# Kernel tuning notes

Measured on AMD Instinct MI355X. Metric: run time of the kernel, lower is better.

Reference implementation:

```python
import jax, jax.numpy as jnp
import numpy as np

IN, H, NCLS = 1280, 128, 263


def _lstm_scan(x_tbd, Wih, Whh, bih, bhh):
    # x_tbd: [T, B, IN]; PyTorch gate order: i, f, g, o. Wih: [4H, IN], Whh: [4H, H]
    B = x_tbd.shape[1]
    b = bih + bhh
    # precompute input projections once: [T, B, 4H]
    xp = jnp.einsum('tbd,gd->tbg', x_tbd, Wih) + b

    def step(carry, xg):
        h, c = carry
        gates = xg + h @ Whh.T
        i, f, g, o = jnp.split(gates, 4, axis=-1)
        i = jax.nn.sigmoid(i)
        f = jax.nn.sigmoid(f)
        g = jnp.tanh(g)
        o = jax.nn.sigmoid(o)
        c = f * c + i * g
        h = o * jnp.tanh(c)
        return (h, c), h

    h0 = jnp.zeros((B, H), x_tbd.dtype)
    c0 = jnp.zeros((B, H), x_tbd.dtype)
    _, hs = jax.lax.scan(step, (h0, c0), xp)
    return hs  # [T, B, H]


def setup_inputs() -> dict:
    key = jax.random.key(0)
    ks = jax.random.split(key, 11)
    s_ih = 1.0 / np.sqrt(H)
    u = lambda k, shape: jax.random.uniform(k, shape, jnp.float32, -s_ih, s_ih)
    return {
        'x': jax.random.normal(ks[0], (64, 512, IN), jnp.float32),
        'Wih_f': u(ks[1], (4 * H, IN)),
        'Whh_f': u(ks[2], (4 * H, H)),
        'bih_f': u(ks[3], (4 * H,)),
        'bhh_f': u(ks[4], (4 * H,)),
        'Wih_b': u(ks[5], (4 * H, IN)),
        'Whh_b': u(ks[6], (4 * H, H)),
        'bih_b': u(ks[7], (4 * H,)),
        'bhh_b': u(ks[8], (4 * H,)),
        'W1': u(ks[9], (NCLS, 2 * H)),
        'b1': u(ks[10], (NCLS,)),
    }


def reference(x, Wih_f, Whh_f, bih_f, bhh_f, Wih_b, Whh_b, bih_b, bhh_b, W1, b1):
    x_tbd = jnp.swapaxes(x, 0, 1)  # [T, B, IN]
    h_f = _lstm_scan(x_tbd, Wih_f, Whh_f, bih_f, bhh_f)           # [T, B, H]
    h_b = _lstm_scan(x_tbd[::-1], Wih_b, Whh_b, bih_b, bhh_b)[::-1]
    h = jnp.concatenate([h_f, h_b], axis=-1)  # [T, B, 2H]
    pooled = jnp.max(h, axis=0)               # temporal max-pool -> [B, 2H]
    # dropout treated as identity (deterministic eval-mode baseline)
    return pooled @ W1.T + b1                  # [B, 263]
```

## Files before the change

kernel.cpp:

```cpp
#include <hip/hip_runtime.h>
#include <hip/hip_bf16.h>

typedef short short8v __attribute__((ext_vector_type(8)));
typedef short short4v __attribute__((ext_vector_type(4)));
typedef float f32x4v __attribute__((ext_vector_type(4)));

#define T_LEN 512
#define BATCH 64
#define INDIM 1280
#define HDIM 128
#define G4 512
#define NCOLS 1024
#define NCLS 263

typedef __attribute__((address_space(1))) const void gvoid_t;
typedef __attribute__((address_space(3))) void lvoid_t;
#define GLOAD_LDS16(g, l) __builtin_amdgcn_global_load_lds((gvoid_t*)(g), (lvoid_t*)(l), 16, 0, 0)

static __device__ __forceinline__ short f2bf(float f) {
    union { float f; unsigned u; } v; v.f = f;
    unsigned r = v.u + 0x7FFF + ((v.u >> 16) & 1);
    return (short)(r >> 16);
}

__global__ void convert_x_kernel(const float4* __restrict__ x, short4v* __restrict__ out, int n4) {
    int i = blockIdx.x * blockDim.x + threadIdx.x;
    int stride = gridDim.x * blockDim.x;
    for (; i < n4; i += stride) {
        float4 v = x[i];
        short4v o;
        o[0] = f2bf(v.x); o[1] = f2bf(v.y); o[2] = f2bf(v.z); o[3] = f2bf(v.w);
        out[i] = o;
    }
}

__global__ void convert_w_kernel(const float* __restrict__ Wf, const float* __restrict__ Wb,
                                 const float* __restrict__ bihf, const float* __restrict__ bhhf,
                                 const float* __restrict__ bihb, const float* __restrict__ bhhb,
                                 short* __restrict__ wout, float* __restrict__ biasc) {
    int i = blockIdx.x * blockDim.x + threadIdx.x;
    int stride = gridDim.x * blockDim.x;
    const int n4 = (G4 * INDIM) / 4;
    for (int k = i; k < 2 * n4; k += stride) {
        const float4* src = (k < n4) ? (const float4*)Wf : (const float4*)Wb;
        float4 v = src[(k < n4) ? k : (k - n4)];
        short4v o;
        o[0] = f2bf(v.x); o[1] = f2bf(v.y); o[2] = f2bf(v.z); o[3] = f2bf(v.w);
        ((short4v*)wout)[k] = o;
    }
    if (i < NCOLS)
        biasc[i] = (i < G4) ? (bihf[i] + bhhf[i]) : (bihb[i - G4] + bhhb[i - G4]);
}

#define BM 128
#define BN 128
#define BK 32

__global__ __launch_bounds__(256) void gemm_xp_kernel(const short* __restrict__ A,
                                                      const short* __restrict__ Bw,
                                                      const float* __restrict__ bias,
                                                      float* __restrict__ C) {
    __shared__ __align__(16) short As[BM * BK];
    __shared__ __align__(16) short Bs[BN * BK];
    const int tid = threadIdx.x;
    const int w = tid >> 6;
    const int l = tid & 63;
    const int bm = blockIdx.x * BM;
    const int bn = blockIdx.y * BN;
    const int wm = (w >> 1) * 64;
    const int wn = (w & 1) * 64;
    const int lr = l & 15;
    const int lk = (l >> 4) * 8;

    f32x4v acc[4][4];
#pragma unroll
    for (int m = 0; m < 4; m++)
#pragma unroll
        for (int n = 0; n < 4; n++) acc[m][n] = (f32x4v)0.0f;

    const int srow = tid >> 2;
    const int scol = (tid & 3) * 8;

#pragma unroll
    for (int i = 0; i < 2; i++) {
        GLOAD_LDS16(A + (long)(bm + i * 64 + srow) * INDIM + scol, &As[(i * 64 + (w << 4)) * BK]);
        GLOAD_LDS16(Bw + (long)(bn + i * 64 + srow) * INDIM + scol, &Bs[(i * 64 + (w << 4)) * BK]);
    }

    for (int k0 = 0; k0 < INDIM; k0 += BK) {
        __syncthreads();
        short8v af[4], bf[4];
#pragma unroll
        for (int m = 0; m < 4; m++) af[m] = *(const short8v*)&As[(wm + m * 16 + lr) * BK + lk];
#pragma unroll
        for (int n = 0; n < 4; n++) bf[n] = *(const short8v*)&Bs[(wn + n * 16 + lr) * BK + lk];
        __syncthreads();
        if (k0 + BK < INDIM) {
            const int k1 = k0 + BK;
#pragma unroll
            for (int i = 0; i < 2; i++) {
                GLOAD_LDS16(A + (long)(bm + i * 64 + srow) * INDIM + k1 + scol, &As[(i * 64 + (w << 4)) * BK]);
                GLOAD_LDS16(Bw + (long)(bn + i * 64 + srow) * INDIM + k1 + scol, &Bs[(i * 64 + (w << 4)) * BK]);
            }
        }
#pragma unroll
        for (int m = 0; m < 4; m++)
#pragma unroll
            for (int n = 0; n < 4; n++)
                acc[m][n] = __builtin_amdgcn_mfma_f32_16x16x32_bf16(af[m], bf[n], acc[m][n], 0, 0, 0);
    }

#pragma unroll
    for (int m = 0; m < 4; m++) {
        const int row = bm + wm + m * 16 + (l >> 4) * 4;
#pragma unroll
        for (int n = 0; n < 4; n++) {
            const int col = bn + wn + n * 16 + lr;
            const float bv = bias[col];
#pragma unroll
            for (int r = 0; r < 4; r++)
                C[(long)(row + r) * NCOLS + col] = acc[m][n][r] + bv;
        }
    }
}

__global__ __launch_bounds__(256, 1) void lstm_rec_kernel(const float* __restrict__ xp,
                                                          const float* __restrict__ Whh_f,
                                                          const float* __restrict__ Whh_b,
                                                          float* __restrict__ pooled) {
    __shared__ __align__(16) short hbf[2][3][136];
    __shared__ __align__(16) float glds[4][2][136];

    const int bid = blockIdx.x;
    const int d = bid & 1;
    const int b0 = (bid >> 1) * 2;
    const int tid = threadIdx.x;
    const int w = tid >> 6;
    const int l = tid & 63;
    const int lr = l & 15;
    const int lg = l >> 4;
    const int lk = lg * 8;
    const int hrow = lr < 2 ? lr : 2;

    const float* __restrict__ Whh = d ? Whh_b : Whh_f;

    short8v afragW[8][4];
#pragma unroll
    for (int nt = 0; nt < 8; nt++) {
        const int gc = w * 128 + nt * 16 + lr;
#pragma unroll
        for (int kk = 0; kk < 4; kk++) {
            const float* src = Whh + gc * HDIM + kk * 32 + lk;
            short8v f;
#pragma unroll
            for (int j = 0; j < 8; j++) f[j] = f2bf(src[j]);
            afragW[nt][kk] = f;
        }
    }

    for (int i = tid; i < 2 * 3 * 136; i += 256) ((short*)hbf)[i] = 0;

    const int eb = tid >> 7;
    const int ec = tid & 127;
    const float* xbase = xp + (long)(b0 + eb) * T_LEN * NCOLS + d * G4 + ec;

    float c = 0.0f;
    float hmax = -1e30f;

#define LOADXV(tq, dst) { \
    int tt_ = d ? (T_LEN - 1 - (tq)) : (tq); \
    tt_ = tt_ < 0 ? 0 : (tt_ > T_LEN - 1 ? T_LEN - 1 : tt_); \
    const float* p_ = xbase + (long)tt_ * NCOLS; \
    _Pragma("unroll") for (int nt_ = 0; nt_ < 4; nt_++) \
        dst[nt_] = p_[nt_ * 128]; \
}

    float xvA[4], xvB[4];
    LOADXV(0, xvA);
    LOADXV(1, xvB);

    __syncthreads();

#define L2E 1.44269504088896f

#define STEP(t, pb, xv) { \
    short8v hfrag[4]; \
    _Pragma("unroll") for (int kk = 0; kk < 4; kk++) \
        hfrag[kk] = *(const short8v*)&hbf[pb][hrow][kk * 32 + lk]; \
    _Pragma("unroll") for (int nt = 0; nt < 8; nt++) { \
        f32x4v a = (f32x4v)0.0f; \
        _Pragma("unroll") for (int kk = 0; kk < 4; kk++) \
            a = __builtin_amdgcn_mfma_f32_16x16x32_bf16(afragW[nt][kk], hfrag[kk], a, 0, 0, 0); \
        if (lr < 2) *(f32x4v*)&glds[w][lr][nt * 16 + lg * 4] = a; \
    } \
    asm volatile("s_waitcnt lgkmcnt(0)\n\ts_barrier" ::: "memory"); \
    { \
        float gi = glds[0][eb][ec] + xv[0]; \
        float gf = glds[1][eb][ec] + xv[1]; \
        float gg = glds[2][eb][ec] + xv[2]; \
        float go = glds[3][eb][ec] + xv[3]; \
        float ea = __builtin_amdgcn_exp2f(-gi * L2E); \
        float eb_ = __builtin_amdgcn_exp2f(-gf * L2E); \
        float pa = 1.0f + ea, pbv = 1.0f + eb_; \
        float inv1 = __builtin_amdgcn_rcpf(pa * pbv); \
        float si = pbv * inv1; \
        float sf = pa * inv1; \
        float eg = __builtin_amdgcn_exp2f(gg * (2.0f * L2E)); \
        float eo = __builtin_amdgcn_exp2f(-go * L2E); \
        float pg = 1.0f + eg, po = 1.0f + eo; \
        float inv2 = __builtin_amdgcn_rcpf(pg * po); \
        float tg = 1.0f - 2.0f * po * inv2; \
        float so = pg * inv2; \
        c = sf * c + si * tg; \
        float ecx = __builtin_amdgcn_exp2f(c * (2.0f * L2E)); \
        float tc = 1.0f - 2.0f * __builtin_amdgcn_rcpf(1.0f + ecx); \
        float h = so * tc; \
        hmax = fmaxf(hmax, h); \
        hbf[(pb) ^ 1][eb][ec] = f2bf(h); \
    } \
    LOADXV((t) + 2, xv); \
    asm volatile("s_waitcnt lgkmcnt(0)\n\ts_barrier" ::: "memory"); \
}

    for (int t = 0; t < T_LEN; t += 2) {
        STEP(t, 0, xvA);
        STEP(t + 1, 1, xvB);
    }

    pooled[(b0 + eb) * 256 + d * 128 + ec] = hmax;
#undef STEP
#undef LOADXV
}

__global__ void logits_kernel(const float* __restrict__ pooled, const float* __restrict__ W1,
                              const float* __restrict__ b1, float* __restrict__ out) {
    __shared__ float p[256];
    const int b = blockIdx.x;
    const int n = threadIdx.x;
    if (n < 256) p[n] = pooled[b * 256 + n];
    __syncthreads();
    if (n < NCLS) {
        float s = b1[n];
        const float* wr = W1 + n * 256;
#pragma unroll 8
        for (int k = 0; k < 256; k++) s += p[k] * wr[k];
        out[b * NCLS + n] = s;
    }
}

extern "C" void kernel_launch(void* const* d_in, const int* in_sizes, int n_in,
                              void* d_out, int out_size, void* d_ws, size_t ws_size,
                              hipStream_t stream) {
    (void)in_sizes; (void)n_in; (void)out_size; (void)ws_size;
    const float* x     = (const float*)d_in[0];
    const float* Wih_f = (const float*)d_in[1];
    const float* Whh_f = (const float*)d_in[2];
    const float* bih_f = (const float*)d_in[3];
    const float* bhh_f = (const float*)d_in[4];
    const float* Wih_b = (const float*)d_in[5];
    const float* Whh_b = (const float*)d_in[6];
    const float* bih_b = (const float*)d_in[7];
    const float* bhh_b = (const float*)d_in[8];
    const float* W1    = (const float*)d_in[9];
    const float* b1    = (const float*)d_in[10];
    float* out = (float*)d_out;

    char* ws = (char*)d_ws;
    short* x_bf   = (short*)ws;
    short* w_bf   = (short*)(ws + 83886080);
    float* biasc  = (float*)(ws + 86507520);
    float* xp     = (float*)(ws + 86511616);
    float* pooled = (float*)(ws + 220729344);

    convert_x_kernel<<<2048, 256, 0, stream>>>((const float4*)x, (short4v*)x_bf, (T_LEN * BATCH * INDIM) / 4);
    convert_w_kernel<<<512, 256, 0, stream>>>(Wih_f, Wih_b, bih_f, bhh_f, bih_b, bhh_b, w_bf, biasc);
    dim3 g(BATCH * T_LEN / BM, NCOLS / BN);
    gemm_xp_kernel<<<g, 256, 0, stream>>>(x_bf, w_bf, biasc, xp);
    lstm_rec_kernel<<<64, 256, 0, stream>>>(xp, Whh_f, Whh_b, pooled);
    logits_kernel<<<64, 320, 0, stream>>>(pooled, W1, b1, out);
}
```

Measured before the change: 504.6 us.

## Remap recurrent gate columns per wave to drop mid-step block barrier

Reassigns the Whh gate columns so that each wave computes all four gates (i,f,g,o) for its own 32 hidden units. The elementwise cell update can then read gate values written by the same wave, and the block-wide barrier between the MFMA phase and the activation phase is removed. The MFMA loop is also reordered to interleave eight independent accumulators across k, which hides MFMA dependency latency. The risk is correctness: intra-wave LDS write-then-read now depends on implicit wave ordering and lgkmcnt waits with no explicit fence.

```diff
diff --git a/kernel.cpp b/kernel.cpp
--- a/kernel.cpp
+++ b/kernel.cpp
@@ -129,7 +129,7 @@
                                                           const float* __restrict__ Whh_b,
                                                           float* __restrict__ pooled) {
     __shared__ __align__(16) short hbf[2][3][136];
-    __shared__ __align__(16) float glds[4][2][136];
+    __shared__ __align__(16) float gw[4][4][2][32];
 
     const int bid = blockIdx.x;
     const int d = bid & 1;
@@ -147,7 +147,7 @@
     short8v afragW[8][4];
 #pragma unroll
     for (int nt = 0; nt < 8; nt++) {
-        const int gc = w * 128 + nt * 16 + lr;
+        const int gc = (nt & 3) * 128 + w * 32 + (nt >> 2) * 16 + lr;
 #pragma unroll
         for (int kk = 0; kk < 4; kk++) {
             const float* src = Whh + gc * HDIM + kk * 32 + lk;
@@ -160,12 +160,14 @@
 
     for (int i = tid; i < 2 * 3 * 136; i += 256) ((short*)hbf)[i] = 0;
 
-    const int eb = tid >> 7;
-    const int ec = tid & 127;
+    const int eb = l >> 5;
+    const int ecl = l & 31;
+    const int ec = w * 32 + ecl;
     const float* xbase = xp + (long)(b0 + eb) * T_LEN * NCOLS + d * G4 + ec;
 
     float c = 0.0f;
     float hmax = -1e30f;
+    const f32x4v z4 = (f32x4v)0.0f;
 
 #define LOADXV(tq, dst) { \
     int tt_ = d ? (T_LEN - 1 - (tq)) : (tq); \
@@ -187,18 +189,21 @@
     short8v hfrag[4]; \
     _Pragma("unroll") for (int kk = 0; kk < 4; kk++) \
         hfrag[kk] = *(const short8v*)&hbf[pb][hrow][kk * 32 + lk]; \
-    _Pragma("unroll") for (int nt = 0; nt < 8; nt++) { \
-        f32x4v a = (f32x4v)0.0f; \
-        _Pragma("unroll") for (int kk = 0; kk < 4; kk++) \
-            a = __builtin_amdgcn_mfma_f32_16x16x32_bf16(afragW[nt][kk], hfrag[kk], a, 0, 0, 0); \
-        if (lr < 2) *(f32x4v*)&glds[w][lr][nt * 16 + lg * 4] = a; \
+    f32x4v acc[8]; \
+    _Pragma("unroll") for (int nt = 0; nt < 8; nt++) \
+        acc[nt] = __builtin_amdgcn_mfma_f32_16x16x32_bf16(afragW[nt][0], hfrag[0], z4, 0, 0, 0); \
+    _Pragma("unroll") for (int kk = 1; kk < 4; kk++) \
+        _Pragma("unroll") for (int nt = 0; nt < 8; nt++) \
+            acc[nt] = __builtin_amdgcn_mfma_f32_16x16x32_bf16(afragW[nt][kk], hfrag[kk], acc[nt], 0, 0, 0); \
+    if (lr < 2) { \
+        _Pragma("unroll") for (int nt = 0; nt < 8; nt++) \
+            *(f32x4v*)&gw[w][nt & 3][lr][(nt >> 2) * 16 + lg * 4] = acc[nt]; \
     } \
-    asm volatile("s_waitcnt lgkmcnt(0)\n\ts_barrier" ::: "memory"); \
     { \
-        float gi = glds[0][eb][ec] + xv[0]; \
-        float gf = glds[1][eb][ec] + xv[1]; \
-        float gg = glds[2][eb][ec] + xv[2]; \
-        float go = glds[3][eb][ec] + xv[3]; \
+        float gi = gw[w][0][eb][ecl] + xv[0]; \
+        float gf = gw[w][1][eb][ecl] + xv[1]; \
+        float gg = gw[w][2][eb][ecl] + xv[2]; \
+        float go = gw[w][3][eb][ecl] + xv[3]; \
         float ea = __builtin_amdgcn_exp2f(-gi * L2E); \
         float eb_ = __builtin_amdgcn_exp2f(-gf * L2E); \
         float pa = 1.0f + ea, pbv = 1.0f + eb_; \
```

Result: no change. 513.1 us (+1.7%).

## Fuse input-projection GEMM with LSTM recurrence using per-tile readiness flags

Applied to the files above, without the earlier changes.

Merges the xp GEMM and the recurrent LSTM kernel into one launch. The first 64 blocks run the recurrence, and the remaining blocks compute GEMM tiles in a time-ordered schedule. Each GEMM block publishes a release-atomic flag when its tile is done. Recurrence blocks poll these flags every 64 steps for the upcoming time window, so the serial recurrence can start before the whole GEMM finishes. The risks are spin-wait overhead, and deadlock or stalls if the recurrence blocks occupy CUs while GEMM tiles are not scheduled. It also adds a memset launch for the flags.

```diff
diff --git a/kernel.cpp b/kernel.cpp
--- a/kernel.cpp
+++ b/kernel.cpp
@@ -56,80 +56,94 @@
 #define BN 128
 #define BK 32
 
-__global__ __launch_bounds__(256) void gemm_xp_kernel(const short* __restrict__ A,
-                                                      const short* __restrict__ Bw,
-                                                      const float* __restrict__ bias,
-                                                      float* __restrict__ C) {
-    __shared__ __align__(16) short As[BM * BK];
-    __shared__ __align__(16) short Bs[BN * BK];
-    const int tid = threadIdx.x;
-    const int w = tid >> 6;
-    const int l = tid & 63;
-    const int bm = blockIdx.x * BM;
-    const int bn = blockIdx.y * BN;
-    const int wm = (w >> 1) * 64;
-    const int wn = (w & 1) * 64;
-    const int lr = l & 15;
-    const int lk = (l >> 4) * 8;
-
-    f32x4v acc[4][4];
-#pragma unroll
-    for (int m = 0; m < 4; m++)
-#pragma unroll
-        for (int n = 0; n < 4; n++) acc[m][n] = (f32x4v)0.0f;
-
-    const int srow = tid >> 2;
-    const int scol = (tid & 3) * 8;
-
-#pragma unroll
-    for (int i = 0; i < 2; i++) {
-        GLOAD_LDS16(A + (long)(bm + i * 64 + srow) * INDIM + scol, &As[(i * 64 + (w << 4)) * BK]);
-        GLOAD_LDS16(Bw + (long)(bn + i * 64 + srow) * INDIM + scol, &Bs[(i * 64 + (w << 4)) * BK]);
-    }
-
-    for (int k0 = 0; k0 < INDIM; k0 += BK) {
-        __syncthreads();
-        short8v af[4], bf[4];
-#pragma unroll
-        for (int m = 0; m < 4; m++) af[m] = *(const short8v*)&As[(wm + m * 16 + lr) * BK + lk];
-#pragma unroll
-        for (int n = 0; n < 4; n++) bf[n] = *(const short8v*)&Bs[(wn + n * 16 + lr) * BK + lk];
-        __syncthreads();
-        if (k0 + BK < INDIM) {
-            const int k1 = k0 + BK;
-#pragma unroll
-            for (int i = 0; i < 2; i++) {
-                GLOAD_LDS16(A + (long)(bm + i * 64 + srow) * INDIM + k1 + scol, &As[(i * 64 + (w << 4)) * BK]);
-                GLOAD_LDS16(Bw + (long)(bn + i * 64 + srow) * INDIM + k1 + scol, &Bs[(i * 64 + (w << 4)) * BK]);
+__global__ __launch_bounds__(256, 1) void fused_gemm_rec_kernel(
+    const short* __restrict__ A, const short* __restrict__ Bw,
+    const float* __restrict__ biasv, float* __restrict__ xp,
+    const float* __restrict__ Whh_f, const float* __restrict__ Whh_b,
+    float* __restrict__ pooled, int* __restrict__ flags) {
+    __shared__ __align__(16) char smem[16384];
+
+    if (blockIdx.x >= 64) {
+        short* As = (short*)smem;
+        short* Bs = (short*)(smem + 8192);
+        const int gid = blockIdx.x - 64;
+        const int chunk = gid >> 8;
+        const int within = gid & 255;
+        const int half = chunk & 1;
+        const int qi = half ? (3 - (chunk >> 1)) : (chunk >> 1);
+        const int gx = (within >> 2) * 4 + qi;
+        const int gy = half * 4 + (within & 3);
+        const int bm = gx * BM;
+        const int bn = gy * BN;
+
+        const int tid = threadIdx.x;
+        const int w = tid >> 6;
+        const int l = tid & 63;
+        const int wm = (w >> 1) * 64;
+        const int wn = (w & 1) * 64;
+        const int lr = l & 15;
+        const int lk = (l >> 4) * 8;
+
+        f32x4v acc[4][4];
+#pragma unroll
+        for (int m = 0; m < 4; m++)
+#pragma unroll
+            for (int n = 0; n < 4; n++) acc[m][n] = (f32x4v)0.0f;
+
+        const int srow = tid >> 2;
+        const int scol = (tid & 3) * 8;
+
+#pragma unroll
+        for (int i = 0; i < 2; i++) {
+            GLOAD_LDS16(A + (long)(bm + i * 64 + srow) * INDIM + scol, &As[(i * 64 + (w << 4)) * BK]);
+            GLOAD_LDS16(Bw + (long)(bn + i * 64 + srow) * INDIM + scol, &Bs[(i * 64 + (w << 4)) * BK]);
+        }
+
+        for (int k0 = 0; k0 < INDIM; k0 += BK) {
+            __syncthreads();
+            short8v af[4], bf[4];
+#pragma unroll
+            for (int m = 0; m < 4; m++) af[m] = *(const short8v*)&As[(wm + m * 16 + lr) * BK + lk];
+#pragma unroll
+            for (int n = 0; n < 4; n++) bf[n] = *(const short8v*)&Bs[(wn + n * 16 + lr) * BK + lk];
+            __syncthreads();
+            if (k0 + BK < INDIM) {
+                const int k1 = k0 + BK;
+#pragma unroll
+                for (int i = 0; i < 2; i++) {
+                    GLOAD_LDS16(A + (long)(bm + i * 64 + srow) * INDIM + k1 + scol, &As[(i * 64 + (w << 4)) * BK]);
+                    GLOAD_LDS16(Bw + (long)(bn + i * 64 + srow) * INDIM + k1 + scol, &Bs[(i * 64 + (w << 4)) * BK]);
+                }
+            }
+#pragma unroll
+            for (int m = 0; m < 4; m++)
+#pragma unroll
+                for (int n = 0; n < 4; n++)
+                    acc[m][n] = __builtin_amdgcn_mfma_f32_16x16x32_bf16(af[m], bf[n], acc[m][n], 0, 0, 0);
+        }
+
+#pragma unroll
+        for (int m = 0; m < 4; m++) {
+            const int row = bm + wm + m * 16 + (l >> 4) * 4;
+#pragma unroll
+            for (int n = 0; n < 4; n++) {
+                const int col = bn + wn + n * 16 + lr;
+                const float bv = biasv[col];
+#pragma unroll
+                for (int r = 0; r < 4; r++)
+                    xp[(long)(row + r) * NCOLS + col] = acc[m][n][r] + bv;
             }
         }
-#pragma unroll
-        for (int m = 0; m < 4; m++)
-#pragma unroll
-            for (int n = 0; n < 4; n++)
-                acc[m][n] = __builtin_amdgcn_mfma_f32_16x16x32_bf16(af[m], bf[n], acc[m][n], 0, 0, 0);
-    }
-
-#pragma unroll
-    for (int m = 0; m < 4; m++) {
-        const int row = bm + wm + m * 16 + (l >> 4) * 4;
-#pragma unroll
-        for (int n = 0; n < 4; n++) {
-            const int col = bn + wn + n * 16 + lr;
-            const float bv = bias[col];
-#pragma unroll
-            for (int r = 0; r < 4; r++)
-                C[(long)(row + r) * NCOLS + col] = acc[m][n][r] + bv;
-        }
-    }
-}
-
-__global__ __launch_bounds__(256, 1) void lstm_rec_kernel(const float* __restrict__ xp,
-                                                          const float* __restrict__ Whh_f,
-                                                          const float* __restrict__ Whh_b,
-                                                          float* __restrict__ pooled) {
-    __shared__ __align__(16) short hbf[2][3][136];
-    __shared__ __align__(16) float glds[4][2][136];
+
+        __threadfence();
+        __syncthreads();
+        if (threadIdx.x == 0)
+            __hip_atomic_fetch_add(&flags[gx * 2 + half], 1, __ATOMIC_RELEASE, __HIP_MEMORY_SCOPE_AGENT);
+        return;
+    }
+
+    short (*hbf)[3][136] = (short (*)[3][136])smem;
+    float (*glds)[2][136] = (float (*)[2][136])(smem + 1632);
 
     const int bid = blockIdx.x;
     const int d = bid & 1;
@@ -158,7 +172,7 @@
         }
     }
 
-    for (int i = tid; i < 2 * 3 * 136; i += 256) ((short*)hbf)[i] = 0;
+    for (int i = tid; i < 2 * 3 * 136; i += 256) ((short*)smem)[i] = 0;
 
     const int eb = tid >> 7;
     const int ec = tid & 127;
@@ -166,6 +180,20 @@
 
     float c = 0.0f;
     float hmax = -1e30f;
+
+#define POLL_WINDOW(t) { \
+    int lo_ = d ? (T_LEN - 1 - (t) - 65) : (t); \
+    int hi_ = d ? (T_LEN - 1 - (t)) : ((t) + 65); \
+    lo_ = lo_ < 0 ? 0 : lo_; hi_ = hi_ > T_LEN - 1 ? T_LEN - 1 : hi_; \
+    const int qa_ = lo_ >> 7, qb_ = hi_ >> 7; \
+    for (int q_ = qa_; q_ <= qb_; ++q_) { \
+        const int f0_ = ((b0) * 4 + q_) * 2 + d; \
+        const int f1_ = ((b0 + 1) * 4 + q_) * 2 + d; \
+        while (__hip_atomic_load(&flags[f0_], __ATOMIC_ACQUIRE, __HIP_MEMORY_SCOPE_AGENT) < 4 || \
+               __hip_atomic_load(&flags[f1_], __ATOMIC_ACQUIRE, __HIP_MEMORY_SCOPE_AGENT) < 4) \
+            __builtin_amdgcn_s_sleep(8); \
+    } \
+}
 
 #define LOADXV(tq, dst) { \
     int tt_ = d ? (T_LEN - 1 - (tq)) : (tq); \
@@ -174,6 +202,8 @@
     _Pragma("unroll") for (int nt_ = 0; nt_ < 4; nt_++) \
         dst[nt_] = p_[nt_ * 128]; \
 }
+
+    POLL_WINDOW(0);
 
     float xvA[4], xvB[4];
     LOADXV(0, xvA);
@@ -223,6 +253,7 @@
 }
 
     for (int t = 0; t < T_LEN; t += 2) {
+        if (t && ((t & 63) == 0)) POLL_WINDOW(t);
         STEP(t, 0, xvA);
         STEP(t + 1, 1, xvB);
     }
@@ -230,6 +261,7 @@
     pooled[(b0 + eb) * 256 + d * 128 + ec] = hmax;
 #undef STEP
 #undef LOADXV
+#undef POLL_WINDOW
 }
 
 __global__ void logits_kernel(const float* __restrict__ pooled, const float* __restrict__ W1,
@@ -271,11 +303,12 @@
     float* biasc  = (float*)(ws + 86507520);
     float* xp     = (float*)(ws + 86511616);
     float* pooled = (float*)(ws + 220729344);
-
+    int*   flags  = (int*)(ws + 220794880);
+
+    hipMemsetAsync(flags, 0, 256 * 2 * sizeof(int), stream);
     convert_x_kernel<<<2048, 256, 0, stream>>>((const float4*)x, (short4v*)x_bf, (T_LEN * BATCH * INDIM) / 4);
     convert_w_kernel<<<512, 256, 0, stream>>>(Wih_f, Wih_b, bih_f, bhh_f, bih_b, bhh_b, w_bf, biasc);
-    dim3 g(BATCH * T_LEN / BM, NCOLS / BN);
-    gemm_xp_kernel<<<g, 256, 0, stream>>>(x_bf, w_bf, biasc, xp);
-    lstm_rec_kernel<<<64, 256, 0, stream>>>(xp, Whh_f, Whh_b, pooled);
+    fused_gemm_rec_kernel<<<64 + 2048, 256, 0, stream>>>(x_bf, w_bf, biasc, xp,
+                                                         Whh_f, Whh_b, pooled, flags);
     logits_kernel<<<64, 320, 0, stream>>>(pooled, W1, b1, out);
 }
```

Result: slower. 1.050 ms (+108.1%).

## Replace input-projection GEMM with 256x256 double-buffered swizzled LDS kernel

Applied to the files above, without the earlier changes.

Rewrites the input-projection GEMM to use 256x256 output tiles with 512 threads, a BK of 64, double-buffered LDS staging via async global-to-LDS loads, an XOR swizzle to avoid bank conflicts, and a remapped block order meant to improve L2 locality. The goal is more operand reuse per loaded byte and overlap of loads with MFMA work. In exchange it uses far more LDS (128KB) and registers, giving one block per CU and only 512 blocks, and it adds manual vmcnt and barrier synchronisation.

```diff
diff --git a/kernel.cpp b/kernel.cpp
--- a/kernel.cpp
+++ b/kernel.cpp
@@ -52,76 +52,112 @@
         biasc[i] = (i < G4) ? (bihf[i] + bhhf[i]) : (bihb[i - G4] + bhhb[i - G4]);
 }
 
-#define BM 128
-#define BN 128
-#define BK 32
-
-__global__ __launch_bounds__(256) void gemm_xp_kernel(const short* __restrict__ A,
-                                                      const short* __restrict__ Bw,
-                                                      const float* __restrict__ bias,
-                                                      float* __restrict__ C) {
-    __shared__ __align__(16) short As[BM * BK];
-    __shared__ __align__(16) short Bs[BN * BK];
+#define NT2 20
+#define NBLK2 512
+
+__global__ __launch_bounds__(512, 1) void gemm256_kernel(const short* __restrict__ A,
+                                                         const short* __restrict__ Bw,
+                                                         const float* __restrict__ bias,
+                                                         float* __restrict__ C) {
+    __shared__ __align__(16) short Ab[2][256 * 64];
+    __shared__ __align__(16) short Bb[2][256 * 64];
+
+    const int orig = blockIdx.x;
+    const int logical = (orig & 7) * (NBLK2 / 8) + (orig >> 3);
+    const int bn = (logical & 3) * 256;
+    const int bm = (logical >> 2) * 256;
+
     const int tid = threadIdx.x;
     const int w = tid >> 6;
     const int l = tid & 63;
-    const int bm = blockIdx.x * BM;
-    const int bn = blockIdx.y * BN;
-    const int wm = (w >> 1) * 64;
-    const int wn = (w & 1) * 64;
     const int lr = l & 15;
-    const int lk = (l >> 4) * 8;
-
-    f32x4v acc[4][4];
-#pragma unroll
-    for (int m = 0; m < 4; m++)
+    const int lg = l >> 4;
+    const int wm2 = (w >> 2) * 128;
+    const int wn2 = (w & 3) * 64;
+
+    int arow[4], scol[4];
+#pragma unroll
+    for (int k = 0; k < 4; k++) {
+        const int cid = k * 512 + tid;
+        arow[k] = cid >> 3;
+        scol[k] = ((cid & 7) ^ (arow[k] & 7)) << 3;
+    }
+    const short* aptr[4];
+    const short* bptr[4];
+#pragma unroll
+    for (int k = 0; k < 4; k++) {
+        aptr[k] = A + (long)(bm + arow[k]) * INDIM + scol[k];
+        bptr[k] = Bw + (long)(bn + arow[k]) * INDIM + scol[k];
+    }
+
+#define STAGE2(kt, b) { \
+    _Pragma("unroll") for (int k_ = 0; k_ < 4; k_++) \
+        GLOAD_LDS16(aptr[k_] + (kt) * 64, &Ab[b][(k_ * 512 + w * 64) * 8]); \
+    _Pragma("unroll") for (int k_ = 0; k_ < 4; k_++) \
+        GLOAD_LDS16(bptr[k_] + (kt) * 64, &Bb[b][(k_ * 512 + w * 64) * 8]); \
+}
+
+    f32x4v acc[8][4];
+#pragma unroll
+    for (int m = 0; m < 8; m++)
 #pragma unroll
         for (int n = 0; n < 4; n++) acc[m][n] = (f32x4v)0.0f;
 
-    const int srow = tid >> 2;
-    const int scol = (tid & 3) * 8;
-
-#pragma unroll
-    for (int i = 0; i < 2; i++) {
-        GLOAD_LDS16(A + (long)(bm + i * 64 + srow) * INDIM + scol, &As[(i * 64 + (w << 4)) * BK]);
-        GLOAD_LDS16(Bw + (long)(bn + i * 64 + srow) * INDIM + scol, &Bs[(i * 64 + (w << 4)) * BK]);
-    }
-
-    for (int k0 = 0; k0 < INDIM; k0 += BK) {
-        __syncthreads();
-        short8v af[4], bf[4];
-#pragma unroll
-        for (int m = 0; m < 4; m++) af[m] = *(const short8v*)&As[(wm + m * 16 + lr) * BK + lk];
-#pragma unroll
-        for (int n = 0; n < 4; n++) bf[n] = *(const short8v*)&Bs[(wn + n * 16 + lr) * BK + lk];
-        __syncthreads();
-        if (k0 + BK < INDIM) {
-            const int k1 = k0 + BK;
-#pragma unroll
-            for (int i = 0; i < 2; i++) {
-                GLOAD_LDS16(A + (long)(bm + i * 64 + srow) * INDIM + k1 + scol, &As[(i * 64 + (w << 4)) * BK]);
-                GLOAD_LDS16(Bw + (long)(bn + i * 64 + srow) * INDIM + k1 + scol, &Bs[(i * 64 + (w << 4)) * BK]);
-            }
+#define FRAG_A(b, row, kk) (*(const short8v*)&Ab[b][(row) * 64 + ((((kk) << 2) + lg) ^ ((row) & 7)) * 8])
+#define FRAG_B(b, row, kk) (*(const short8v*)&Bb[b][(row) * 64 + ((((kk) << 2) + lg) ^ ((row) & 7)) * 8])
+
+#define COMPUTE2(b) { \
+    short8v bfr[4][2]; \
+    _Pragma("unroll") for (int nf = 0; nf < 4; nf++) { \
+        const int brow = wn2 + nf * 16 + lr; \
+        bfr[nf][0] = FRAG_B(b, brow, 0); \
+        bfr[nf][1] = FRAG_B(b, brow, 1); \
+    } \
+    _Pragma("unroll") for (int mf = 0; mf < 8; mf++) { \
+        const int amrow = wm2 + mf * 16 + lr; \
+        short8v af0 = FRAG_A(b, amrow, 0); \
+        short8v af1 = FRAG_A(b, amrow, 1); \
+        _Pragma("unroll") for (int nf = 0; nf < 4; nf++) { \
+            acc[mf][nf] = __builtin_amdgcn_mfma_f32_16x16x32_bf16(af0, bfr[nf][0], acc[mf][nf], 0, 0, 0); \
+            acc[mf][nf] = __builtin_amdgcn_mfma_f32_16x16x32_bf16(af1, bfr[nf][1], acc[mf][nf], 0, 0, 0); \
+        } \
+    } \
+}
+
+    STAGE2(0, 0);
+    STAGE2(1, 1);
+
+    for (int t = 0; t < NT2 - 2; ++t) {
+        asm volatile("s_waitcnt vmcnt(8)" ::: "memory");
+        __builtin_amdgcn_s_barrier();
+        if (t & 1) { COMPUTE2(1); } else { COMPUTE2(0); }
+        __builtin_amdgcn_s_barrier();
+        if (t & 1) { STAGE2(t + 2, 1); } else { STAGE2(t + 2, 0); }
+    }
+    asm volatile("s_waitcnt vmcnt(8)" ::: "memory");
+    __builtin_amdgcn_s_barrier();
+    COMPUTE2(0);
+    __builtin_amdgcn_s_barrier();
+    asm volatile("s_waitcnt vmcnt(0)" ::: "memory");
+    __builtin_amdgcn_s_barrier();
+    COMPUTE2(1);
+
+#pragma unroll
+    for (int nf = 0; nf < 4; nf++) {
+        const int col = bn + wn2 + nf * 16 + lr;
+        const float bv = bias[col];
+#pragma unroll
+        for (int mf = 0; mf < 8; mf++) {
+            const int row = bm + wm2 + mf * 16 + lg * 4;
+#pragma unroll
+            for (int r = 0; r < 4; r++)
+                C[(long)(row + r) * NCOLS + col] = acc[mf][nf][r] + bv;
         }
-#pragma unroll
-        for (int m = 0; m < 4; m++)
-#pragma unroll
-            for (int n = 0; n < 4; n++)
-                acc[m][n] = __builtin_amdgcn_mfma_f32_16x16x32_bf16(af[m], bf[n], acc[m][n], 0, 0, 0);
-    }
-
-#pragma unroll
-    for (int m = 0; m < 4; m++) {
-        const int row = bm + wm + m * 16 + (l >> 4) * 4;
-#pragma unroll
-        for (int n = 0; n < 4; n++) {
-            const int col = bn + wn + n * 16 + lr;
-            const float bv = bias[col];
-#pragma unroll
-            for (int r = 0; r < 4; r++)
-                C[(long)(row + r) * NCOLS + col] = acc[m][n][r] + bv;
-        }
-    }
+    }
+#undef STAGE2
+#undef COMPUTE2
+#undef FRAG_A
+#undef FRAG_B
 }
 
 __global__ __launch_bounds__(256, 1) void lstm_rec_kernel(const float* __restrict__ xp,
@@ -274,8 +310,7 @@
 
     convert_x_kernel<<<2048, 256, 0, stream>>>((const float4*)x, (short4v*)x_bf, (T_LEN * BATCH * INDIM) / 4);
     convert_w_kernel<<<512, 256, 0, stream>>>(Wih_f, Wih_b, bih_f, bhh_f, bih_b, bhh_b, w_bf, biasc);
-    dim3 g(BATCH * T_LEN / BM, NCOLS / BN);
-    gemm_xp_kernel<<<g, 256, 0, stream>>>(x_bf, w_bf, biasc, xp);
+    gemm256_kernel<<<NBLK2, 512, 0, stream>>>(x_bf, w_bf, biasc, xp);
     lstm_rec_kernel<<<64, 256, 0, stream>>>(xp, Whh_f, Whh_b, pooled);
     logits_kernel<<<64, 320, 0, stream>>>(pooled, W1, b1, out);
 }
```

After: 676.1 us. +34.0%, slower.
